# Kernel tuning notes

Hardware: AMD Instinct MI355X
Metric: run time of the kernel (lower is better)

## Reference

```python
import jax, jax.numpy as jnp
import numpy as np

N = 100000      # nodes
E = 1600000     # edges (avg degree 16)
D_IN = 128
D_OUT = 64
N_SCALES = 3
DEPTH = 10
TELEPORTS = np.array([0.1, 0.2, 0.3], dtype=np.float32)


def setup_inputs() -> dict:
    key = jax.random.key(0)
    ks = jax.random.split(key, 9)
    data = jax.random.normal(ks[0], (N, D_IN), dtype=jnp.float32)
    src = jax.random.randint(ks[1], (E,), 0, N, dtype=jnp.int32)
    tgt = jax.random.randint(ks[2], (E,), 0, N, dtype=jnp.int32)
    s = 1.0 / np.sqrt(D_IN)
    Ws = jax.random.uniform(ks[3], (N_SCALES, D_IN, D_OUT), jnp.float32, -s, s)
    bs = jax.random.uniform(ks[4], (N_SCALES, D_OUT), jnp.float32, -s, s)
    W_src = jax.random.uniform(ks[5], (D_IN, D_OUT), jnp.float32, -s, s)
    b_src = jax.random.uniform(ks[6], (D_OUT,), jnp.float32, -s, s)
    so = 1.0 / np.sqrt(D_OUT)
    W_tgt = jax.random.uniform(ks[7], (D_OUT, D_OUT), jnp.float32, -so, so)
    b_tgt = jax.random.uniform(ks[8], (D_OUT,), jnp.float32, -so, so)
    return {"data": data, "src": src, "tgt": tgt, "Ws": Ws, "bs": bs,
            "W_src": W_src, "b_src": b_src, "W_tgt": W_tgt, "b_tgt": b_tgt}


def reference(data, src, tgt, Ws, bs, W_src, b_src, W_tgt, b_tgt):
    # per-target-node degree (indices.unique counts repeated per edge)
    deg = jax.ops.segment_sum(jnp.ones((E,), jnp.float32), tgt, num_segments=N)
    deg_inv = 1.0 / jnp.maximum(deg, 1.0)           # [N]
    edge_w = deg_inv[tgt][:, None]                  # [E,1] normalized factor

    def laplacian(x):                               # x: [N, D_OUT]
        diff = (x[tgt] - x[src]) * edge_w           # (own - source_message)/deg
        return jax.ops.segment_sum(diff, tgt, num_segments=N)

    lap3 = jax.vmap(laplacian)                      # over scale dim

    t = jnp.asarray(TELEPORTS)[:, None, None]       # [S,1,1]
    emb = jnp.einsum('nd,sdo->sno', data, Ws) + bs[:, None, :]   # [S,N,O]
    out = emb
    for _ in range(DEPTH):
        out = (1.0 - t) * lap3(out) + t * emb
    scales = jax.nn.relu(out)                       # [S,N,O]

    s_att = data @ W_src + b_src                    # [N,O]
    t_att = jnp.einsum('sno,op->snp', scales, W_tgt) + b_tgt     # [S,N,O]
    logits = jnp.einsum('snp,np->sn', t_att, s_att)              # [S,N]
    att = jax.nn.softmax(logits, axis=0)            # softmax over scales
    return jnp.einsum('sn,sno->no', att, scales)    # [N,O]
```

## Files before the change

kernel.cpp:

```cpp
#include <hip/hip_runtime.h>
#include <hip/hip_bf16.h>

#define NN   100000
#define EE   1600000
#define CAP  48
#define NT   6250

typedef __attribute__((ext_vector_type(8))) short bf16x8;
typedef __attribute__((ext_vector_type(4))) float f32x4;

__device__ inline short f2b_rne(float f) {
  union { float f; unsigned u; } x; x.f = f;
  unsigned r = x.u + 0x7fffu + ((x.u >> 16) & 1u);
  return (short)(r >> 16);
}
__device__ inline unsigned pack_rne(float lo, float hi) {
  unsigned ul = __float_as_uint(lo); ul += 0x7fffu + ((ul >> 16) & 1u);
  unsigned uh = __float_as_uint(hi); uh += 0x7fffu + ((uh >> 16) & 1u);
  return __builtin_amdgcn_perm(uh, ul, 0x07060302u);
}
__device__ inline float lo2f(unsigned u) { return __uint_as_float(u << 16); }
__device__ inline float hi2f(unsigned u) { return __uint_as_float(u & 0xffff0000u); }

__global__ void k_fill(const int* __restrict__ tgt, const int* __restrict__ src,
                       int* __restrict__ cnt, int* __restrict__ col) {
  int e = blockIdx.x * 256 + threadIdx.x;
  if (e >= EE) return;
  int t = tgt[e];
  int p = atomicAdd(&cnt[t], 1);
  if (p < CAP) col[t * CAP + p] = src[e];
}

__global__ void k_cast(const float* __restrict__ data, unsigned* __restrict__ y0) {
  int i = blockIdx.x * 256 + threadIdx.x;
  const float2 v = ((const float2*)data)[i];
  y0[i] = pack_rne(v.x, v.y);
}

template <int MODE>
__global__ __launch_bounds__(256) void k_prop(
    const int* __restrict__ cnt, const int* __restrict__ col,
    const unsigned* __restrict__ xin, unsigned* __restrict__ xout,
    unsigned* __restrict__ z0, unsigned* __restrict__ z1,
    unsigned* __restrict__ z2,
    float ca0, float ca1, float ca2, float cb0, float cb1, float cb2) {
  const int wv = threadIdx.x >> 6, lane = threadIdx.x & 63;
  const int n = blockIdx.x * 4 + wv;
  if (n >= NN) return;
  const int d = cnt[n];
  const int dm = (d < CAP) ? d : CAP;
  int idx = (lane < dm) ? col[n * CAP + lane] : 0;
  const unsigned own = xin[(size_t)n * 64 + lane];
  float s0 = 0.f, s1 = 0.f;
  int i = 0;
  for (; i + 4 <= dm; i += 4) {
    int ja = __shfl(idx, i),     jb = __shfl(idx, i + 1);
    int jc = __shfl(idx, i + 2), jd = __shfl(idx, i + 3);
    unsigned a = xin[(size_t)ja * 64 + lane];
    unsigned b = xin[(size_t)jb * 64 + lane];
    unsigned c = xin[(size_t)jc * 64 + lane];
    unsigned e = xin[(size_t)jd * 64 + lane];
    s0 += (lo2f(a) + lo2f(b)) + (lo2f(c) + lo2f(e));
    s1 += (hi2f(a) + hi2f(b)) + (hi2f(c) + hi2f(e));
  }
  for (; i < dm; ++i) {
    int j = __shfl(idx, i);
    unsigned a = xin[(size_t)j * 64 + lane];
    s0 += lo2f(a); s1 += hi2f(a);
  }
  const float gate = (d > 0) ? 1.f : 0.f;
  const float inv  = (d > 0) ? 1.f / (float)d : 0.f;
  const float o0 = lo2f(own), o1 = hi2f(own);
  const float l0 = gate * (o0 - inv * s0);
  const float l1 = gate * (o1 - inv * s1);
  const size_t p = (size_t)n * 64 + lane;
  if (MODE != 3) xout[p] = pack_rne(l0, l1);
  if (MODE == 1) {
    z0[p] = pack_rne(ca0 * o0 + cb0 * l0, ca0 * o1 + cb0 * l1);
    z1[p] = pack_rne(ca1 * o0 + cb1 * l0, ca1 * o1 + cb1 * l1);
    z2[p] = pack_rne(ca2 * o0 + cb2 * l0, ca2 * o1 + cb2 * l1);
  } else if (MODE == 2) {
    unsigned u0 = z0[p], u1 = z1[p], u2 = z2[p];
    z0[p] = pack_rne(lo2f(u0) + ca0 * o0 + cb0 * l0, hi2f(u0) + ca0 * o1 + cb0 * l1);
    z1[p] = pack_rne(lo2f(u1) + ca1 * o0 + cb1 * l0, hi2f(u1) + ca1 * o1 + cb1 * l1);
    z2[p] = pack_rne(lo2f(u2) + ca2 * o0 + cb2 * l0, hi2f(u2) + ca2 * o1 + cb2 * l1);
  } else if (MODE == 3) {
    unsigned u0 = z0[p], u1 = z1[p], u2 = z2[p];
    z0[p] = pack_rne(lo2f(u0) + cb0 * l0, hi2f(u0) + cb0 * l1);
    z1[p] = pack_rne(lo2f(u1) + cb1 * l0, hi2f(u1) + cb1 * l1);
    z2[p] = pack_rne(lo2f(u2) + cb2 * l0, hi2f(u2) + cb2 * l1);
  }
}

__global__ __launch_bounds__(256) void k_gemm2(
    const unsigned* __restrict__ z0, const unsigned* __restrict__ z1,
    const unsigned* __restrict__ z2, const unsigned* __restrict__ y0,
    const float* __restrict__ Ws, const float* __restrict__ bs,
    const float* __restrict__ Wsrc, const float* __restrict__ bsrc,
    __hip_bfloat16* __restrict__ scales, float* __restrict__ satt) {
  const int lane = threadIdx.x & 63;
  const int wv   = threadIdx.x >> 6;
  const int n16  = lane & 15;
  const int q    = lane >> 4;
  const unsigned* Ab = (wv == 0) ? z0 : (wv == 1) ? z1 : (wv == 2) ? z2 : y0;
  const float tw = 0.1f * (float)(wv + 1);

  bf16x8 Bf[4][4];
  float  bias[4];
#pragma unroll
  for (int ct = 0; ct < 4; ++ct) {
    const int c = ct * 16 + n16;
    const float* bp = (wv < 3) ? (Ws + (size_t)wv * 8192 + c) : (Wsrc + c);
    bias[ct] = (wv < 3) ? tw * bs[wv * 64 + c] : bsrc[c];
#pragma unroll
    for (int s = 0; s < 4; ++s) {
      const int k0 = s * 32 + q * 8;
      union { short h[8]; bf16x8 v; } u;
#pragma unroll
      for (int j = 0; j < 8; ++j) u.h[j] = f2b_rne(bp[(size_t)(k0 + j) * 64]);
      Bf[ct][s] = u.v;
    }
  }

  for (int t = blockIdx.x; t < NT; t += gridDim.x) {
    const int row = t * 16 + n16;
    const uint4* ap = (const uint4*)(Ab + (size_t)row * 64);
    f32x4 acc[4];
#pragma unroll
    for (int ct = 0; ct < 4; ++ct)
      acc[ct] = (f32x4){bias[ct], bias[ct], bias[ct], bias[ct]};
#pragma unroll
    for (int s = 0; s < 4; ++s) {
      union { uint4 u; bf16x8 v; } af;
      af.u = ap[s * 4 + q];
#pragma unroll
      for (int ct = 0; ct < 4; ++ct)
        acc[ct] = __builtin_amdgcn_mfma_f32_16x16x32_bf16(af.v, Bf[ct][s], acc[ct], 0, 0, 0);
    }
    if (wv < 3) {
#pragma unroll
      for (int ct = 0; ct < 4; ++ct) {
        const int c = wv * 64 + ct * 16 + n16;
#pragma unroll
        for (int i = 0; i < 4; ++i) {
          const int r = t * 16 + q * 4 + i;
          scales[(size_t)r * 192 + c] = __float2bfloat16(acc[ct][i]);
        }
      }
    } else {
#pragma unroll
      for (int ct = 0; ct < 4; ++ct) {
        const int c = ct * 16 + n16;
#pragma unroll
        for (int i = 0; i < 4; ++i) {
          const int r = t * 16 + q * 4 + i;
          satt[(size_t)r * 64 + c] = acc[ct][i];
        }
      }
    }
  }
}

__global__ __launch_bounds__(256) void k_att(
    const __hip_bfloat16* __restrict__ scales, const float* __restrict__ Wt,
    float* __restrict__ io) {
  __shared__ float WT[64 * 64];
  const int tid = threadIdx.x;
  for (int i = tid; i < 4096; i += 256) WT[(i & 63) * 64 + (i >> 6)] = Wt[i];
  __syncthreads();
  const int wv = tid >> 6, lane = tid & 63;
  for (int n = blockIdx.x * 4 + wv; n < NN; n += gridDim.x * 4) {
    const __hip_bfloat16* sr = scales + (size_t)n * 192;
    float v0 = fmaxf(__bfloat162float(sr[lane]), 0.f);
    float v1 = fmaxf(__bfloat162float(sr[64 + lane]), 0.f);
    float v2 = fmaxf(__bfloat162float(sr[128 + lane]), 0.f);
    float a = io[(size_t)n * 64 + lane];
    float m = 0.f;
#pragma unroll
    for (int p = 0; p < 64; ++p) m = fmaf(WT[p * 64 + lane], __shfl(a, p), m);
    float l0 = v0 * m, l1 = v1 * m, l2 = v2 * m;
#pragma unroll
    for (int off = 32; off; off >>= 1) {
      l0 += __shfl_xor(l0, off);
      l1 += __shfl_xor(l1, off);
      l2 += __shfl_xor(l2, off);
    }
    float mx = fmaxf(l0, fmaxf(l1, l2));
    float x0 = __expf(l0 - mx), x1 = __expf(l1 - mx), x2 = __expf(l2 - mx);
    float invs = 1.f / (x0 + x1 + x2);
    io[(size_t)n * 64 + lane] = (x0 * v0 + x1 * v1 + x2 * v2) * invs;
  }
}

extern "C" void kernel_launch(void* const* d_in, const int* in_sizes, int n_in,
                              void* d_out, int out_size, void* d_ws, size_t ws_size,
                              hipStream_t stream) {
  (void)in_sizes; (void)n_in; (void)out_size; (void)ws_size;
  const float* data = (const float*)d_in[0];
  const int*   srcp = (const int*)d_in[1];
  const int*   tgtp = (const int*)d_in[2];
  const float* Ws   = (const float*)d_in[3];
  const float* bs   = (const float*)d_in[4];
  const float* Wsrc = (const float*)d_in[5];
  const float* bsrc = (const float*)d_in[6];
  const float* Wtgt = (const float*)d_in[7];
  float* out = (float*)d_out;

  char* ws = (char*)d_ws;
  auto al = [](size_t x) { return (x + 255) & ~(size_t)255; };
  const size_t o_col = al((size_t)NN * 4);
  const size_t o_y0  = o_col + al((size_t)NN * CAP * 4);
  const size_t szY   = al((size_t)NN * 64 * 4);
  int*      cnt = (int*)ws;
  int*      col = (int*)(ws + o_col);
  unsigned* Y0  = (unsigned*)(ws + o_y0);
  unsigned* Ya  = (unsigned*)(ws + o_y0 + szY);
  unsigned* Yb  = (unsigned*)(ws + o_y0 + 2 * szY);
  unsigned* z0  = (unsigned*)(ws + o_y0 + 3 * szY);
  unsigned* z1  = (unsigned*)(ws + o_y0 + 4 * szY);
  unsigned* z2  = (unsigned*)(ws + o_y0 + 5 * szY);
  __hip_bfloat16* scales = (__hip_bfloat16*)(ws + o_y0 + 6 * szY);

  float c[3][11];
  for (int s = 0; s < 3; ++s) {
    float t = 0.1f * (float)(s + 1), p = 1.f;
    for (int j = 0; j < 10; ++j) { c[s][j] = t * p; p *= (1.f - t); }
    c[s][10] = p;
  }

  hipMemsetAsync(cnt, 0, NN * sizeof(int), stream);
  k_fill<<<(EE + 255) / 256, 256, 0, stream>>>(tgtp, srcp, cnt, col);
  k_cast<<<NN * 64 / 256, 256, 0, stream>>>(data, Y0);

  const int PG = (NN + 3) / 4;
  k_prop<1><<<PG, 256, 0, stream>>>(cnt, col, Y0, Ya, z0, z1, z2,
      c[0][0], c[1][0], c[2][0], c[0][1], c[1][1], c[2][1]);
  k_prop<0><<<PG, 256, 0, stream>>>(cnt, col, Ya, Yb, nullptr, nullptr, nullptr,
      0, 0, 0, 0, 0, 0);
  k_prop<2><<<PG, 256, 0, stream>>>(cnt, col, Yb, Ya, z0, z1, z2,
      c[0][2], c[1][2], c[2][2], c[0][3], c[1][3], c[2][3]);
  k_prop<0><<<PG, 256, 0, stream>>>(cnt, col, Ya, Yb, nullptr, nullptr, nullptr,
      0, 0, 0, 0, 0, 0);
  k_prop<2><<<PG, 256, 0, stream>>>(cnt, col, Yb, Ya, z0, z1, z2,
      c[0][4], c[1][4], c[2][4], c[0][5], c[1][5], c[2][5]);
  k_prop<0><<<PG, 256, 0, stream>>>(cnt, col, Ya, Yb, nullptr, nullptr, nullptr,
      0, 0, 0, 0, 0, 0);
  k_prop<2><<<PG, 256, 0, stream>>>(cnt, col, Yb, Ya, z0, z1, z2,
      c[0][6], c[1][6], c[2][6], c[0][7], c[1][7], c[2][7]);
  k_prop<0><<<PG, 256, 0, stream>>>(cnt, col, Ya, Yb, nullptr, nullptr, nullptr,
      0, 0, 0, 0, 0, 0);
  k_prop<2><<<PG, 256, 0, stream>>>(cnt, col, Yb, Ya, z0, z1, z2,
      c[0][8], c[1][8], c[2][8], c[0][9], c[1][9], c[2][9]);
  k_prop<3><<<PG, 256, 0, stream>>>(cnt, col, Ya, Yb, z0, z1, z2,
      0, 0, 0, c[0][10], c[1][10], c[2][10]);

  k_gemm2<<<512, 256, 0, stream>>>(z0, z1, z2, Y0, Ws, bs, Wsrc, bsrc, scales, out);
  k_att<<<2048, 256, 0, stream>>>(scales, Wtgt, out);
}
```

Before: 1.071 ms.

## Bucket-partition CSR build and batch z accumulation across propagation steps

Replaces the single atomic-scatter adjacency fill with a three-phase build: histogram edges into node buckets, scan the histogram, partition the edges, then build per-bucket CSR in shared memory and write it out coalesced. The propagation schedule also keeps several Laplacian iterates live in rotating buffers. The z0..z2 accumulators are then updated only at three points, using four-coefficient combinations, instead of after every second step. This cuts scattered global atomics and repeated read-modify-write traffic on the three accumulators. In exchange it adds a partition buffer, extra launches and extra per-node reads of saved iterates.

```diff
diff --git a/kernel.cpp b/kernel.cpp
--- a/kernel.cpp
+++ b/kernel.cpp
@@ -5,6 +5,8 @@
 #define EE   1600000
 #define CAP  48
 #define NT   6250
+#define NPB  192
+#define NB   521
 
 typedef __attribute__((ext_vector_type(8))) short bf16x8;
 typedef __attribute__((ext_vector_type(4))) float f32x4;
@@ -22,13 +24,102 @@
 __device__ inline float lo2f(unsigned u) { return __uint_as_float(u << 16); }
 __device__ inline float hi2f(unsigned u) { return __uint_as_float(u & 0xffff0000u); }
 
-__global__ void k_fill(const int* __restrict__ tgt, const int* __restrict__ src,
-                       int* __restrict__ cnt, int* __restrict__ col) {
-  int e = blockIdx.x * 256 + threadIdx.x;
-  if (e >= EE) return;
-  int t = tgt[e];
-  int p = atomicAdd(&cnt[t], 1);
-  if (p < CAP) col[t * CAP + p] = src[e];
+__global__ __launch_bounds__(256) void k_fillA(const int* __restrict__ tgt,
+                                               int* __restrict__ ghist) {
+  __shared__ int h[NB];
+  for (int i = threadIdx.x; i < NB; i += 256) h[i] = 0;
+  __syncthreads();
+  int e = blockIdx.x * 4096 + threadIdx.x;
+#pragma unroll
+  for (int k = 0; k < 16; ++k, e += 256)
+    if (e < EE) atomicAdd(&h[tgt[e] / NPB], 1);
+  __syncthreads();
+  for (int i = threadIdx.x; i < NB; i += 256)
+    if (h[i]) atomicAdd(&ghist[i], h[i]);
+}
+
+__global__ __launch_bounds__(256) void k_scan(const int* __restrict__ ghist,
+                                              int* __restrict__ base,
+                                              int* __restrict__ tail) {
+  __shared__ int v[1024];
+  const int tid = threadIdx.x;
+  for (int i = tid; i < 1024; i += 256) v[i] = (i < NB) ? ghist[i] : 0;
+  __syncthreads();
+  for (int off = 1; off < 1024; off <<= 1) {
+    int tmp[4];
+#pragma unroll
+    for (int j = 0; j < 4; ++j) {
+      int i = tid + j * 256;
+      tmp[j] = (i >= off) ? v[i - off] : 0;
+    }
+    __syncthreads();
+#pragma unroll
+    for (int j = 0; j < 4; ++j) v[tid + j * 256] += tmp[j];
+    __syncthreads();
+  }
+  for (int i = tid; i <= NB; i += 256) {
+    int bb = (i == 0) ? 0 : v[i - 1];
+    base[i] = bb;
+    if (i < NB) tail[i] = bb;
+  }
+}
+
+__global__ __launch_bounds__(256) void k_fillB(const int* __restrict__ tgt,
+                                               const int* __restrict__ src,
+                                               int* tail, uint2* __restrict__ part) {
+  __shared__ int hist[NB], cur[NB], basel[NB];
+  const int tid = threadIdx.x;
+  for (int i = tid; i < NB; i += 256) { hist[i] = 0; cur[i] = 0; }
+  __syncthreads();
+  const int e0 = blockIdx.x * 4096 + tid;
+  int tv[16], sv[16];
+#pragma unroll
+  for (int k = 0; k < 16; ++k) {
+    int e = e0 + k * 256;
+    tv[k] = -1;
+    if (e < EE) {
+      tv[k] = tgt[e]; sv[k] = src[e];
+      atomicAdd(&hist[tv[k] / NPB], 1);
+    }
+  }
+  __syncthreads();
+  for (int b = tid; b < NB; b += 256)
+    if (hist[b]) basel[b] = atomicAdd(&tail[b], hist[b]);
+  __syncthreads();
+#pragma unroll
+  for (int k = 0; k < 16; ++k) {
+    if (tv[k] >= 0) {
+      int b = tv[k] / NPB;
+      int r = atomicAdd(&cur[b], 1);
+      part[basel[b] + r] = make_uint2((unsigned)sv[k], (unsigned)tv[k]);
+    }
+  }
+}
+
+__global__ __launch_bounds__(256) void k_fillC(const int* __restrict__ base,
+                                               const uint2* __restrict__ part,
+                                               int* __restrict__ cnt,
+                                               int* __restrict__ col) {
+  __shared__ int ccnt[NPB];
+  __shared__ int ccol[NPB * CAP];
+  const int b = blockIdx.x, tid = threadIdx.x;
+  for (int i = tid; i < NPB; i += 256) ccnt[i] = 0;
+  __syncthreads();
+  const int lo = base[b], hi = base[b + 1];
+  for (int i = lo + tid; i < hi; i += 256) {
+    uint2 e = part[i];
+    int nl = (int)e.y - b * NPB;
+    int p = atomicAdd(&ccnt[nl], 1);
+    if (p < CAP) ccol[nl * CAP + p] = (int)e.x;
+  }
+  __syncthreads();
+  const int n0 = b * NPB;
+  for (int i = tid; i < NPB; i += 256)
+    if (n0 + i < NN) cnt[n0 + i] = ccnt[i];
+  for (int i = tid; i < NPB * CAP; i += 256) {
+    int n = n0 + i / CAP;
+    if (n < NN) col[(size_t)n0 * CAP + i] = ccol[i];
+  }
 }
 
 __global__ void k_cast(const float* __restrict__ data, unsigned* __restrict__ y0) {
@@ -40,17 +131,24 @@
 template <int MODE>
 __global__ __launch_bounds__(256) void k_prop(
     const int* __restrict__ cnt, const int* __restrict__ col,
-    const unsigned* __restrict__ xin, unsigned* __restrict__ xout,
+    const unsigned* __restrict__ xin, unsigned* xout,
+    const unsigned* s0p, const unsigned* s1p,
     unsigned* __restrict__ z0, unsigned* __restrict__ z1,
     unsigned* __restrict__ z2,
-    float ca0, float ca1, float ca2, float cb0, float cb1, float cb2) {
+    float4 g0, float4 g1, float4 g2) {
   const int wv = threadIdx.x >> 6, lane = threadIdx.x & 63;
   const int n = blockIdx.x * 4 + wv;
   if (n >= NN) return;
+  const size_t p = (size_t)n * 64 + lane;
   const int d = cnt[n];
   const int dm = (d < CAP) ? d : CAP;
   int idx = (lane < dm) ? col[n * CAP + lane] : 0;
-  const unsigned own = xin[(size_t)n * 64 + lane];
+  const unsigned own = xin[p];
+  unsigned S0 = 0, S1 = 0, U0 = 0, U1 = 0, U2 = 0;
+  if (MODE == 1 || MODE == 2 || MODE == 3) S0 = s0p[p];
+  if (MODE == 1 || MODE == 2) S1 = s1p[p];
+  if (MODE == 2 || MODE == 3) { U0 = z0[p]; U1 = z1[p]; U2 = z2[p]; }
+
   float s0 = 0.f, s1 = 0.f;
   int i = 0;
   for (; i + 4 <= dm; i += 4) {
@@ -73,22 +171,31 @@
   const float o0 = lo2f(own), o1 = hi2f(own);
   const float l0 = gate * (o0 - inv * s0);
   const float l1 = gate * (o1 - inv * s1);
-  const size_t p = (size_t)n * 64 + lane;
   if (MODE != 3) xout[p] = pack_rne(l0, l1);
-  if (MODE == 1) {
-    z0[p] = pack_rne(ca0 * o0 + cb0 * l0, ca0 * o1 + cb0 * l1);
-    z1[p] = pack_rne(ca1 * o0 + cb1 * l0, ca1 * o1 + cb1 * l1);
-    z2[p] = pack_rne(ca2 * o0 + cb2 * l0, ca2 * o1 + cb2 * l1);
-  } else if (MODE == 2) {
-    unsigned u0 = z0[p], u1 = z1[p], u2 = z2[p];
-    z0[p] = pack_rne(lo2f(u0) + ca0 * o0 + cb0 * l0, hi2f(u0) + ca0 * o1 + cb0 * l1);
-    z1[p] = pack_rne(lo2f(u1) + ca1 * o0 + cb1 * l0, hi2f(u1) + ca1 * o1 + cb1 * l1);
-    z2[p] = pack_rne(lo2f(u2) + ca2 * o0 + cb2 * l0, hi2f(u2) + ca2 * o1 + cb2 * l1);
+  if (MODE == 1 || MODE == 2) {
+    const float a0 = lo2f(S0), a1 = hi2f(S0), b0 = lo2f(S1), b1 = hi2f(S1);
+    float t0lo = g0.x * a0 + g0.y * b0 + g0.z * o0 + g0.w * l0;
+    float t0hi = g0.x * a1 + g0.y * b1 + g0.z * o1 + g0.w * l1;
+    float t1lo = g1.x * a0 + g1.y * b0 + g1.z * o0 + g1.w * l0;
+    float t1hi = g1.x * a1 + g1.y * b1 + g1.z * o1 + g1.w * l1;
+    float t2lo = g2.x * a0 + g2.y * b0 + g2.z * o0 + g2.w * l0;
+    float t2hi = g2.x * a1 + g2.y * b1 + g2.z * o1 + g2.w * l1;
+    if (MODE == 2) {
+      t0lo += lo2f(U0); t0hi += hi2f(U0);
+      t1lo += lo2f(U1); t1hi += hi2f(U1);
+      t2lo += lo2f(U2); t2hi += hi2f(U2);
+    }
+    z0[p] = pack_rne(t0lo, t0hi);
+    z1[p] = pack_rne(t1lo, t1hi);
+    z2[p] = pack_rne(t2lo, t2hi);
   } else if (MODE == 3) {
-    unsigned u0 = z0[p], u1 = z1[p], u2 = z2[p];
-    z0[p] = pack_rne(lo2f(u0) + cb0 * l0, hi2f(u0) + cb0 * l1);
-    z1[p] = pack_rne(lo2f(u1) + cb1 * l0, hi2f(u1) + cb1 * l1);
-    z2[p] = pack_rne(lo2f(u2) + cb2 * l0, hi2f(u2) + cb2 * l1);
+    const float a0 = lo2f(S0), a1 = hi2f(S0);
+    z0[p] = pack_rne(lo2f(U0) + g0.x * a0 + g0.z * o0 + g0.w * l0,
+                     hi2f(U0) + g0.x * a1 + g0.z * o1 + g0.w * l1);
+    z1[p] = pack_rne(lo2f(U1) + g1.x * a0 + g1.z * o0 + g1.w * l0,
+                     hi2f(U1) + g1.x * a1 + g1.z * o1 + g1.w * l1);
+    z2[p] = pack_rne(lo2f(U2) + g2.x * a0 + g2.z * o0 + g2.w * l0,
+                     hi2f(U2) + g2.x * a1 + g2.z * o1 + g2.w * l1);
   }
 }
 
@@ -208,51 +315,67 @@
 
   char* ws = (char*)d_ws;
   auto al = [](size_t x) { return (x + 255) & ~(size_t)255; };
-  const size_t o_col = al((size_t)NN * 4);
-  const size_t o_y0  = o_col + al((size_t)NN * CAP * 4);
-  const size_t szY   = al((size_t)NN * 64 * 4);
-  int*      cnt = (int*)ws;
-  int*      col = (int*)(ws + o_col);
-  unsigned* Y0  = (unsigned*)(ws + o_y0);
-  unsigned* Ya  = (unsigned*)(ws + o_y0 + szY);
-  unsigned* Yb  = (unsigned*)(ws + o_y0 + 2 * szY);
-  unsigned* z0  = (unsigned*)(ws + o_y0 + 3 * szY);
-  unsigned* z1  = (unsigned*)(ws + o_y0 + 4 * szY);
-  unsigned* z2  = (unsigned*)(ws + o_y0 + 5 * szY);
-  __hip_bfloat16* scales = (__hip_bfloat16*)(ws + o_y0 + 6 * szY);
+  size_t off = 0;
+  auto take = [&](size_t bytes) { size_t o = off; off += al(bytes); return o; };
+  int*      cnt   = (int*)(ws + take((size_t)NN * 4));
+  int*      col   = (int*)(ws + take((size_t)NN * CAP * 4));
+  int*      ghist = (int*)(ws + take((size_t)NB * 4));
+  int*      base  = (int*)(ws + take((size_t)(NB + 1) * 4));
+  int*      tail  = (int*)(ws + take((size_t)NB * 4));
+  uint2*    part  = (uint2*)(ws + take((size_t)EE * 8));
+  const size_t szY = (size_t)NN * 64 * 4;
+  unsigned* Y0 = (unsigned*)(ws + take(szY));
+  unsigned* R1 = (unsigned*)(ws + take(szY));
+  unsigned* R2 = (unsigned*)(ws + take(szY));
+  unsigned* R3 = (unsigned*)(ws + take(szY));
+  unsigned* z0 = (unsigned*)(ws + take(szY));
+  unsigned* z1 = (unsigned*)(ws + take(szY));
+  unsigned* z2 = (unsigned*)(ws + take(szY));
+  __hip_bfloat16* scales = (__hip_bfloat16*)R2;
 
   float c[3][11];
   for (int s = 0; s < 3; ++s) {
-    float t = 0.1f * (float)(s + 1), p = 1.f;
-    for (int j = 0; j < 10; ++j) { c[s][j] = t * p; p *= (1.f - t); }
-    c[s][10] = p;
-  }
-
-  hipMemsetAsync(cnt, 0, NN * sizeof(int), stream);
-  k_fill<<<(EE + 255) / 256, 256, 0, stream>>>(tgtp, srcp, cnt, col);
+    float t = 0.1f * (float)(s + 1), pw = 1.f;
+    for (int j = 0; j < 10; ++j) { c[s][j] = t * pw; pw *= (1.f - t); }
+    c[s][10] = pw;
+  }
+  float4 A3[3], A7[3], A10[3];
+  for (int s = 0; s < 3; ++s) {
+    A3[s]  = make_float4(c[s][0], c[s][1], c[s][2], c[s][3]);
+    A7[s]  = make_float4(c[s][4], c[s][5], c[s][6], c[s][7]);
+    A10[s] = make_float4(c[s][8], 0.f,     c[s][9], c[s][10]);
+  }
+  const float4 Zf = make_float4(0.f, 0.f, 0.f, 0.f);
+
+  const int EB = (EE + 4095) / 4096;
+  hipMemsetAsync(ghist, 0, NB * 4, stream);
+  k_fillA<<<EB, 256, 0, stream>>>(tgtp, ghist);
+  k_scan<<<1, 256, 0, stream>>>(ghist, base, tail);
+  k_fillB<<<EB, 256, 0, stream>>>(tgtp, srcp, tail, part);
+  k_fillC<<<NB, 256, 0, stream>>>(base, part, cnt, col);
   k_cast<<<NN * 64 / 256, 256, 0, stream>>>(data, Y0);
 
   const int PG = (NN + 3) / 4;
-  k_prop<1><<<PG, 256, 0, stream>>>(cnt, col, Y0, Ya, z0, z1, z2,
-      c[0][0], c[1][0], c[2][0], c[0][1], c[1][1], c[2][1]);
-  k_prop<0><<<PG, 256, 0, stream>>>(cnt, col, Ya, Yb, nullptr, nullptr, nullptr,
-      0, 0, 0, 0, 0, 0);
-  k_prop<2><<<PG, 256, 0, stream>>>(cnt, col, Yb, Ya, z0, z1, z2,
-      c[0][2], c[1][2], c[2][2], c[0][3], c[1][3], c[2][3]);
-  k_prop<0><<<PG, 256, 0, stream>>>(cnt, col, Ya, Yb, nullptr, nullptr, nullptr,
-      0, 0, 0, 0, 0, 0);
-  k_prop<2><<<PG, 256, 0, stream>>>(cnt, col, Yb, Ya, z0, z1, z2,
-      c[0][4], c[1][4], c[2][4], c[0][5], c[1][5], c[2][5]);
-  k_prop<0><<<PG, 256, 0, stream>>>(cnt, col, Ya, Yb, nullptr, nullptr, nullptr,
-      0, 0, 0, 0, 0, 0);
-  k_prop<2><<<PG, 256, 0, stream>>>(cnt, col, Yb, Ya, z0, z1, z2,
-      c[0][6], c[1][6], c[2][6], c[0][7], c[1][7], c[2][7]);
-  k_prop<0><<<PG, 256, 0, stream>>>(cnt, col, Ya, Yb, nullptr, nullptr, nullptr,
-      0, 0, 0, 0, 0, 0);
-  k_prop<2><<<PG, 256, 0, stream>>>(cnt, col, Yb, Ya, z0, z1, z2,
-      c[0][8], c[1][8], c[2][8], c[0][9], c[1][9], c[2][9]);
-  k_prop<3><<<PG, 256, 0, stream>>>(cnt, col, Ya, Yb, z0, z1, z2,
-      0, 0, 0, c[0][10], c[1][10], c[2][10]);
+  k_prop<0><<<PG, 256, 0, stream>>>(cnt, col, Y0, R1, nullptr, nullptr,
+      nullptr, nullptr, nullptr, Zf, Zf, Zf);
+  k_prop<0><<<PG, 256, 0, stream>>>(cnt, col, R1, R2, nullptr, nullptr,
+      nullptr, nullptr, nullptr, Zf, Zf, Zf);
+  k_prop<1><<<PG, 256, 0, stream>>>(cnt, col, R2, R3, Y0, R1,
+      z0, z1, z2, A3[0], A3[1], A3[2]);
+  k_prop<0><<<PG, 256, 0, stream>>>(cnt, col, R3, R1, nullptr, nullptr,
+      nullptr, nullptr, nullptr, Zf, Zf, Zf);
+  k_prop<0><<<PG, 256, 0, stream>>>(cnt, col, R1, R2, nullptr, nullptr,
+      nullptr, nullptr, nullptr, Zf, Zf, Zf);
+  k_prop<0><<<PG, 256, 0, stream>>>(cnt, col, R2, R3, nullptr, nullptr,
+      nullptr, nullptr, nullptr, Zf, Zf, Zf);
+  k_prop<2><<<PG, 256, 0, stream>>>(cnt, col, R3, R1, R1, R2,
+      z0, z1, z2, A7[0], A7[1], A7[2]);
+  k_prop<0><<<PG, 256, 0, stream>>>(cnt, col, R1, R2, nullptr, nullptr,
+      nullptr, nullptr, nullptr, Zf, Zf, Zf);
+  k_prop<0><<<PG, 256, 0, stream>>>(cnt, col, R2, R3, nullptr, nullptr,
+      nullptr, nullptr, nullptr, Zf, Zf, Zf);
+  k_prop<3><<<PG, 256, 0, stream>>>(cnt, col, R3, nullptr, R2, nullptr,
+      z0, z1, z2, A10[0], A10[1], A10[2]);
 
   k_gemm2<<<512, 256, 0, stream>>>(z0, z1, z2, Y0, Ws, bs, Wsrc, bsrc, scales, out);
   k_att<<<2048, 256, 0, stream>>>(scales, Wtgt, out);
```

After: 972.4 us. -9.2%, faster.
